# Kernel optimization log

Hardware: AMD Instinct MI355X
Metric: run time of the kernel (lower is better)

The kernel has to match this reference:

```python
import jax, jax.numpy as jnp
import numpy as np

N_ENTITY = 200000
N_RELATIONS = 32
DIM = 64
N_HOP = 2
N_MEMORY = 32
BATCH = 1024
KGE_WEIGHT = 0.01
L2_WEIGHT = 1e-7


def setup_inputs() -> dict:
    key = jax.random.key(0)
    ks = jax.random.split(key, 8)
    items = jax.random.randint(ks[0], (BATCH,), 0, N_ENTITY)
    labels = jax.random.uniform(ks[1], (BATCH,), dtype=jnp.float32)
    memories_h = jax.random.randint(ks[2], (N_HOP, BATCH, N_MEMORY), 0, N_ENTITY)
    memories_r = jax.random.randint(ks[3], (N_HOP, BATCH, N_MEMORY), 0, N_RELATIONS)
    memories_t = jax.random.randint(ks[4], (N_HOP, BATCH, N_MEMORY), 0, N_ENTITY)
    item_table = jax.random.normal(ks[5], (N_ENTITY, DIM), dtype=jnp.float32) * 0.1
    relation_table = jax.random.normal(ks[6], (N_RELATIONS, DIM * DIM), dtype=jnp.float32) * 0.1
    transform_W = jax.random.normal(ks[7], (DIM, DIM), dtype=jnp.float32) * 0.1
    return dict(items=items, labels=labels, memories_h=memories_h,
                memories_r=memories_r, memories_t=memories_t,
                item_table=item_table, relation_table=relation_table,
                transform_W=transform_W)


def _forward(items, labels, memories_h, memories_r, memories_t,
             item_table, relation_table, transform_W):
    v = item_table[items]  # [B, D]
    o_list = []
    kge_loss = jnp.float32(0.0)
    l2_loss = jnp.float32(0.0)
    for hop in range(N_HOP):
        h = item_table[memories_h[hop]]                                   # [B, M, D]
        R = relation_table[memories_r[hop]].reshape(-1, N_MEMORY, DIM, DIM)  # [B, M, D, D]
        t = item_table[memories_t[hop]]                                   # [B, M, D]
        # Rh = R @ h  -> [B, M, D]
        Rh = jnp.einsum('bmij,bmj->bmi', R, h)
        # attention probs over memory slots
        probs = jax.nn.softmax(jnp.einsum('bmi,bi->bm', Rh, v), axis=-1)  # [B, M]
        o = jnp.einsum('bmd,bm->bd', t, probs)                            # [B, D]
        # item_update_mode == 'plus_transform': v = W(v + o)
        v = (v + o) @ transform_W.T
        o_list.append(o)
        # KGE loss: sigmoid(h^T R t), mean over [B, M]
        hRt = jnp.einsum('bmi,bmij,bmj->bm', h, R, t)
        kge_loss = kge_loss + jnp.mean(jax.nn.sigmoid(hRt))
        l2_loss = l2_loss + jnp.sum(h * h) + jnp.sum(t * t) + jnp.sum(R * R)
    kge_loss = -KGE_WEIGHT * kge_loss
    l2_loss = L2_WEIGHT * l2_loss
    # predict with all hops
    y = o_list[-1]
    for i in range(N_HOP - 1):
        y = y + o_list[i]
    scores = jax.nn.sigmoid(jnp.sum(v * y, axis=1))  # [B]
    # BCE loss (torch clamps log at -100)
    logp = jnp.clip(jnp.log(scores), -100.0)
    lognp = jnp.clip(jnp.log(1.0 - scores), -100.0)
    base_loss = -jnp.mean(labels * logp + (1.0 - labels) * lognp)
    loss = base_loss + kge_loss + l2_loss
    return scores, loss, base_loss, kge_loss, l2_loss


def reference(items, labels, memories_h, memories_r, memories_t,
              item_table, relation_table, transform_W):
    return _forward(items, labels, memories_h, memories_r, memories_t,
                    item_table, relation_table, transform_W)
```

## Files before the change

### kernel.cpp

```cpp
#include <hip/hip_runtime.h>
#include <math.h>

#define N_ENTITY 200000
#define N_REL 32
#define DIM 64
#define N_HOP 2
#define N_MEM 32
#define BATCH 1024
#define PAIR_PER_HOP (BATCH * N_MEM)
#define N_PAIR (N_HOP * PAIR_PER_HOP)
#define CAP 3072
#define JBLK 32
#define WPB 4
#define NBLK_PAIRS (JBLK * N_REL * WPB)
#define TPAD 68

typedef __attribute__((ext_vector_type(8))) short short8;
typedef __attribute__((ext_vector_type(4))) float floatx4;

__device__ __forceinline__ float wave_reduce_sum(float v) {
    v += __shfl_xor(v, 1);
    v += __shfl_xor(v, 2);
    v += __shfl_xor(v, 4);
    v += __shfl_xor(v, 8);
    v += __shfl_xor(v, 16);
    v += __shfl_xor(v, 32);
    return v;
}

__device__ __forceinline__ unsigned short f2b(float x) {
    union { float f; unsigned u; } c; c.f = x;
    const unsigned r = (c.u + 0x7FFFu + ((c.u >> 16) & 1u)) >> 16;
    return (unsigned short)r;
}

__device__ __forceinline__ float b2f(short s) {
    union { unsigned u; float f; } c;
    c.u = ((unsigned)(unsigned short)s) << 16;
    return c.f;
}

__device__ __forceinline__ short8 pack8(const float4 a, const float4 b) {
    short8 s;
    s[0] = (short)f2b(a.x); s[1] = (short)f2b(a.y);
    s[2] = (short)f2b(a.z); s[3] = (short)f2b(a.w);
    s[4] = (short)f2b(b.x); s[5] = (short)f2b(b.y);
    s[6] = (short)f2b(b.z); s[7] = (short)f2b(b.w);
    return s;
}

__device__ __forceinline__ float sq4(const float4 a) {
    return a.x * a.x + a.y * a.y + a.z * a.z + a.w * a.w;
}

__device__ __forceinline__ float dot4(const float4 a, const float4 b) {
    return a.x * b.x + a.y * b.y + a.z * b.z + a.w * b.w;
}

__global__ __launch_bounds__(256) void ripple_bin(
    const int* __restrict__ mr,
    int* __restrict__ g_cnt,
    int* __restrict__ list)
{
    __shared__ int hist[N_REL];
    __shared__ int cur[N_REL];
    const int tid = (int)threadIdx.x;
    const int pbase = (int)blockIdx.x * 1024;

    if (tid < N_REL) hist[tid] = 0;
    __syncthreads();

    int rv[4];
    #pragma unroll
    for (int u = 0; u < 4; ++u) {
        rv[u] = mr[pbase + u * 256 + tid];
        atomicAdd(&hist[rv[u]], 1);
    }
    __syncthreads();
    if (tid < N_REL) cur[tid] = atomicAdd(&g_cnt[tid], hist[tid]);
    __syncthreads();
    #pragma unroll
    for (int u = 0; u < 4; ++u) {
        const int r = rv[u];
        const int pos = atomicAdd(&cur[r], 1);
        if (pos < CAP) list[r * CAP + pos] = pbase + u * 256 + tid;
    }
}

__global__ __launch_bounds__(256) void ripple_pairs(
    const int* __restrict__ items,
    const int* __restrict__ mh,
    const int* __restrict__ mt,
    const float* __restrict__ item_table,
    const float* __restrict__ rel_table,
    const int* __restrict__ g_cnt,
    const int* __restrict__ list,
    float* __restrict__ wsL,
    unsigned short* __restrict__ wsRh,
    float* __restrict__ ws_kge,
    float* __restrict__ ws_l2)
{
    __shared__ __align__(16) float sTr[WPB][16 * TPAD];
    __shared__ __align__(16) short8 sB[512];
    __shared__ float sRed[WPB];

    const int tid = (int)threadIdx.x;
    const int lane = tid & 63;
    const int w = tid >> 6;
    const int j = (int)blockIdx.x;
    const int r = (int)blockIdx.y;
    const int n = min(g_cnt[r], CAP);

    const int m16 = lane & 15;
    const int quad = lane >> 4;
    const int rb = r * CAP;
    const int wave_id = j * WPB + w;

    float* __restrict__ buf = &sTr[w][0];

    int tau = wave_id;
    int p = 0, hidx = 0, tidx = 0, iidx = 0;
    if (tau * 16 < n) {
        const int pos = min(tau * 16 + m16, n - 1);
        p = list[rb + pos];
        hidx = mh[p];
        tidx = mt[p];
        iidx = (p < PAIR_PER_HOP) ? items[p >> 5] : 0;
    }

    {
        const float* __restrict__ Rb = rel_table + (size_t)r * (DIM * DIM);
        float rsq = 0.f;
        #pragma unroll
        for (int u = 0; u < 2; ++u) {
            const int slot = tid + 256 * u;
            const int s = slot >> 8;
            const int tn = (slot >> 6) & 3;
            const int ls = slot & 63;
            const float* src = Rb + (size_t)(16 * tn + (ls & 15)) * DIM
                             + 32 * s + 8 * (ls >> 4);
            const float4 a = *(const float4*)src;
            const float4 b = *(const float4*)(src + 4);
            rsq += sq4(a) + sq4(b);
            sB[slot] = pack8(a, b);
        }
        rsq = wave_reduce_sum(rsq);
        if (lane == 0) sRed[w] = rsq;
    }
    __syncthreads();
    const float Rsum = sRed[0] + sRed[1] + sRed[2] + sRed[3];

    short8 Bf[2][4];
    #pragma unroll
    for (int s = 0; s < 2; ++s)
        #pragma unroll
        for (int tn = 0; tn < 4; ++tn)
            Bf[s][tn] = sB[s * 256 + tn * 64 + lane];

    float kge = 0.f;
    float l2ht = 0.f;
    int cnt = 0;

    for (; tau * 16 < n; tau += JBLK * WPB) {
        const int base = tau * 16;
        const bool mvalid = (base + m16) < n;
        const bool hop0 = p < PAIR_PER_HOP;

        const float* __restrict__ hp = item_table + (size_t)hidx * DIM + 8 * quad;
        const float* __restrict__ tp = item_table + (size_t)tidx * DIM + 8 * quad;
        const float4 h0a = *(const float4*)hp;
        const float4 h0b = *(const float4*)(hp + 4);
        const float4 h1a = *(const float4*)(hp + 32);
        const float4 h1b = *(const float4*)(hp + 36);
        const float4 t0a = *(const float4*)tp;
        const float4 t0b = *(const float4*)(tp + 4);
        const float4 t1a = *(const float4*)(tp + 32);
        const float4 t1b = *(const float4*)(tp + 36);

        float4 va0, va1, va2, va3;
        va0 = va1 = va2 = va3 = make_float4(0.f, 0.f, 0.f, 0.f);
        if (hop0) {
            const float* __restrict__ vp =
                item_table + (size_t)iidx * DIM + 16 * quad;
            va0 = *(const float4*)vp;
            va1 = *(const float4*)(vp + 4);
            va2 = *(const float4*)(vp + 8);
            va3 = *(const float4*)(vp + 12);
        }

        const int tau2 = tau + JBLK * WPB;
        int p2 = 0, h2 = 0, t2 = 0, i2 = 0;
        if (tau2 * 16 < n) {
            const int pos2 = min(tau2 * 16 + m16, n - 1);
            p2 = list[rb + pos2];
            h2 = mh[p2];
            t2 = mt[p2];
            i2 = (p2 < PAIR_PER_HOP) ? items[p2 >> 5] : 0;
        }

        if (mvalid) {
            l2ht += sq4(h0a) + sq4(h0b) + sq4(h1a) + sq4(h1b)
                  + sq4(t0a) + sq4(t0b) + sq4(t1a) + sq4(t1b);
        }

        const short8 Ah0 = pack8(h0a, h0b);
        const short8 Ah1 = pack8(h1a, h1b);
        const short8 At0 = pack8(t0a, t0b);
        const short8 At1 = pack8(t1a, t1b);

        floatx4 Ch[4], Ct[4];
        const floatx4 z4 = {0.f, 0.f, 0.f, 0.f};
        #pragma unroll
        for (int tn = 0; tn < 4; ++tn) {
            Ch[tn] = __builtin_amdgcn_mfma_f32_16x16x32_bf16(Ah0, Bf[0][tn], z4, 0, 0, 0);
            Ch[tn] = __builtin_amdgcn_mfma_f32_16x16x32_bf16(Ah1, Bf[1][tn], Ch[tn], 0, 0, 0);
            Ct[tn] = __builtin_amdgcn_mfma_f32_16x16x32_bf16(At0, Bf[0][tn], z4, 0, 0, 0);
            Ct[tn] = __builtin_amdgcn_mfma_f32_16x16x32_bf16(At1, Bf[1][tn], Ct[tn], 0, 0, 0);
        }

        #pragma unroll
        for (int tn = 0; tn < 4; ++tn) {
            const int col = m16 + 16 * tn;
            #pragma unroll
            for (int q = 0; q < 4; ++q)
                buf[(4 * quad + q) * TPAD + col] = Ct[tn][q];
        }
        const float* rowT = buf + m16 * TPAD;
        const float4 ct0 = *(const float4*)(rowT + 8 * quad);
        const float4 ct1 = *(const float4*)(rowT + 8 * quad + 4);
        const float4 ct2 = *(const float4*)(rowT + 32 + 8 * quad);
        const float4 ct3 = *(const float4*)(rowT + 32 + 8 * quad + 4);
        float hrt = dot4(h0a, ct0) + dot4(h0b, ct1) + dot4(h1a, ct2) + dot4(h1b, ct3);
        hrt += __shfl_xor(hrt, 16);
        hrt += __shfl_xor(hrt, 32);

        #pragma unroll
        for (int tn = 0; tn < 4; ++tn) {
            const int col = m16 + 16 * tn;
            #pragma unroll
            for (int q = 0; q < 4; ++q)
                buf[(4 * quad + q) * TPAD + col] = Ch[tn][q];
        }
        const float* rowC = buf + m16 * TPAD;
        const float4 c0 = *(const float4*)(rowC + 16 * quad);
        const float4 c1 = *(const float4*)(rowC + 16 * quad + 4);
        const float4 c2 = *(const float4*)(rowC + 16 * quad + 8);
        const float4 c3 = *(const float4*)(rowC + 16 * quad + 12);

        float lg = dot4(va0, c0) + dot4(va1, c1) + dot4(va2, c2) + dot4(va3, c3);
        lg += __shfl_xor(lg, 16);
        lg += __shfl_xor(lg, 32);

        if (quad == 0 && mvalid) {
            kge += 1.f / (1.f + expf(-hrt));
            if (hop0) wsL[p] = lg;
        }

        if (mvalid && !hop0) {
            unsigned short* __restrict__ dst =
                wsRh + (size_t)(p - PAIR_PER_HOP) * DIM + 16 * quad;
            *(short8*)dst = pack8(c0, c1);
            *(short8*)(dst + 8) = pack8(c2, c3);
        }

        cnt += min(16, n - base);
        p = p2; hidx = h2; tidx = t2; iidx = i2;
    }

    const float l2tot = wave_reduce_sum(l2ht) + (float)cnt * Rsum;
    const float kgetot = wave_reduce_sum(kge);
    if (lane == 0) {
        const int bid = (r * JBLK + j) * WPB + w;
        ws_kge[bid] = kgetot;
        ws_l2[bid] = l2tot;
    }
}

__global__ __launch_bounds__(256) void ripple_attn(
    const int* __restrict__ items,
    const float* __restrict__ labels,
    const int* __restrict__ mt,
    const float* __restrict__ item_table,
    const float* __restrict__ W,
    const float* __restrict__ wsL,
    const unsigned short* __restrict__ wsRh,
    float* __restrict__ out,
    float* __restrict__ ws_bce)
{
    __shared__ __align__(16) float sV[4][DIM];

    const int tid = (int)threadIdx.x;
    const int lane = tid & 63;
    const int w = tid >> 6;
    const int b = (int)blockIdx.x * 4 + w;

    const float v0 = item_table[(size_t)items[b] * DIM + lane];

    const float lab = labels[b];

    float l0 = (lane < N_MEM) ? wsL[b * N_MEM + lane] : -1e30f;

    const int myidx = mt[(lane >> 5) * PAIR_PER_HOP + b * N_MEM + (lane & 31)];

    float treg[64];
    #pragma unroll
    for (int m = 0; m < 64; ++m) {
        const int idx = __shfl(myidx, m);
        treg[m] = item_table[(size_t)idx * DIM + lane];
    }

    const int m1 = lane >> 1;
    const int d1 = (lane & 1) * 32;
    short8 rv[4];
    #pragma unroll
    for (int e = 0; e < 4; ++e)
        rv[e] = *(const short8*)(wsRh + (size_t)(b * N_MEM + m1) * DIM + d1 + 8 * e);

    const float4* __restrict__ Wrow = (const float4*)(W + (size_t)lane * DIM);

    float mx = l0;
    #pragma unroll
    for (int d = 16; d >= 1; d >>= 1) mx = fmaxf(mx, __shfl_xor(mx, d));
    const float e0 = expf(l0 - mx);
    float se = (lane < N_MEM) ? e0 : 0.f;
    #pragma unroll
    for (int d = 16; d >= 1; d >>= 1) se += __shfl_xor(se, d);
    const float pe0 = e0 / se;

    float o0 = 0.f;
    #pragma unroll
    for (int m = 0; m < N_MEM; ++m)
        o0 = fmaf(treg[m], __shfl(pe0, m), o0);

    sV[w][lane] = v0 + o0;
    float v1;
    {
        float a0 = 0.f, a1 = 0.f, a2 = 0.f, a3 = 0.f;
        #pragma unroll
        for (int k = 0; k < 16; ++k) {
            const float4 w4 = Wrow[k];
            const float4 u4 = *(const float4*)&sV[w][k * 4];
            a0 = fmaf(w4.x, u4.x, a0);
            a1 = fmaf(w4.y, u4.y, a1);
            a2 = fmaf(w4.z, u4.z, a2);
            a3 = fmaf(w4.w, u4.w, a3);
        }
        v1 = (a0 + a1) + (a2 + a3);
    }

    sV[w][lane] = v1;
    float dp = 0.f;
    #pragma unroll
    for (int e = 0; e < 4; ++e) {
        const float4 va = *(const float4*)&sV[w][d1 + 8 * e];
        const float4 vb = *(const float4*)&sV[w][d1 + 8 * e + 4];
        dp += b2f(rv[e][0]) * va.x + b2f(rv[e][1]) * va.y
            + b2f(rv[e][2]) * va.z + b2f(rv[e][3]) * va.w
            + b2f(rv[e][4]) * vb.x + b2f(rv[e][5]) * vb.y
            + b2f(rv[e][6]) * vb.z + b2f(rv[e][7]) * vb.w;
    }
    dp += __shfl_xor(dp, 1);
    const float a1v = __shfl(dp, (lane & 31) * 2);

    float av = (lane < N_MEM) ? a1v : -1e30f;
    mx = av;
    #pragma unroll
    for (int d = 16; d >= 1; d >>= 1) mx = fmaxf(mx, __shfl_xor(mx, d));
    const float e1 = expf(av - mx);
    se = (lane < N_MEM) ? e1 : 0.f;
    #pragma unroll
    for (int d = 16; d >= 1; d >>= 1) se += __shfl_xor(se, d);
    const float pe1 = e1 / se;

    float o1 = 0.f;
    #pragma unroll
    for (int m = 0; m < N_MEM; ++m)
        o1 = fmaf(treg[N_MEM + m], __shfl(pe1, m), o1);

    const float y = o0 + o1;
    sV[w][lane] = v1 + o1;
    float v2;
    {
        float a0 = 0.f, a1_ = 0.f, a2 = 0.f, a3 = 0.f;
        #pragma unroll
        for (int k = 0; k < 16; ++k) {
            const float4 w4 = Wrow[k];
            const float4 u4 = *(const float4*)&sV[w][k * 4];
            a0 = fmaf(w4.x, u4.x, a0);
            a1_ = fmaf(w4.y, u4.y, a1_);
            a2 = fmaf(w4.z, u4.z, a2);
            a3 = fmaf(w4.w, u4.w, a3);
        }
        v2 = (a0 + a1_) + (a2 + a3);
    }

    float s = wave_reduce_sum(v2 * y);
    s = 1.f / (1.f + expf(-s));
    if (lane == 0) {
        out[b] = s;
        const float logp = fmaxf(logf(s), -100.f);
        const float lognp = fmaxf(logf(1.f - s), -100.f);
        ws_bce[b] = lab * logp + (1.f - lab) * lognp;
    }
}

__global__ __launch_bounds__(256) void ripple_finalize(
    const float* __restrict__ ws_bce,
    const float* __restrict__ ws_kge,
    const float* __restrict__ ws_l2,
    float* __restrict__ out)
{
    __shared__ float sb[4], sk[4], sl[4];
    const int tid = (int)threadIdx.x;
    float bsum = 0.f, ksum = 0.f, lsum = 0.f;
    for (int i = tid; i < BATCH; i += 256) bsum += ws_bce[i];
    for (int i = tid; i < NBLK_PAIRS; i += 256) {
        ksum += ws_kge[i];
        lsum += ws_l2[i];
    }
    bsum = wave_reduce_sum(bsum);
    ksum = wave_reduce_sum(ksum);
    lsum = wave_reduce_sum(lsum);
    const int w = tid >> 6;
    if ((tid & 63) == 0) { sb[w] = bsum; sk[w] = ksum; sl[w] = lsum; }
    __syncthreads();
    if (tid == 0) {
        const float bs = sb[0] + sb[1] + sb[2] + sb[3];
        const float ks = sk[0] + sk[1] + sk[2] + sk[3];
        const float ls = sl[0] + sl[1] + sl[2] + sl[3];
        const float base_loss = -bs / (float)BATCH;
        const float kge_loss = -0.01f * (ks / (float)(BATCH * N_MEM));
        const float l2_loss = 1e-7f * ls;
        out[BATCH + 0] = base_loss + kge_loss + l2_loss;
        out[BATCH + 1] = base_loss;
        out[BATCH + 2] = kge_loss;
        out[BATCH + 3] = l2_loss;
    }
}

extern "C" void kernel_launch(void* const* d_in, const int* in_sizes, int n_in,
                              void* d_out, int out_size, void* d_ws, size_t ws_size,
                              hipStream_t stream) {
    const int* items        = (const int*)d_in[0];
    const float* labels     = (const float*)d_in[1];
    const int* mh           = (const int*)d_in[2];
    const int* mr           = (const int*)d_in[3];
    const int* mt           = (const int*)d_in[4];
    const float* item_table = (const float*)d_in[5];
    const float* rel_table  = (const float*)d_in[6];
    const float* W          = (const float*)d_in[7];
    float* out = (float*)d_out;

    float* ws = (float*)d_ws;
    float* wsL            = ws;
    unsigned short* wsRh  = (unsigned short*)(wsL + PAIR_PER_HOP);
    int*   list           = (int*)(wsRh + (size_t)PAIR_PER_HOP * DIM);
    int*   g_cnt          = list + N_REL * CAP;
    float* ws_bce         = (float*)(g_cnt + N_REL);
    float* ws_kge         = ws_bce + BATCH;
    float* ws_l2          = ws_kge + NBLK_PAIRS;

    hipMemsetAsync(g_cnt, 0, N_REL * sizeof(int), stream);
    ripple_bin<<<N_PAIR / 1024, 256, 0, stream>>>(mr, g_cnt, list);
    dim3 gpairs(JBLK, N_REL);
    ripple_pairs<<<gpairs, 256, 0, stream>>>(items, mh, mt, item_table, rel_table,
                                             g_cnt, list, wsL, wsRh, ws_kge, ws_l2);
    ripple_attn<<<BATCH / 4, 256, 0, stream>>>(items, labels, mt, item_table, W,
                                               wsL, wsRh, out, ws_bce);
    ripple_finalize<<<1, 256, 0, stream>>>(ws_bce, ws_kge, ws_l2, out);
}
```

Measured before the change: 132.4 us.

## Fold relation binning into pairs kernel and finalize via last-block atomics

Drops the separate binning kernel. Each pairs block now scans a fixed 2048-pair segment and collects, in shared memory, the pairs whose relation matches its block row. The finalize kernel is also removed: the attention kernel adds BCE terms atomically, and the last block to finish computes the loss outputs. This cuts kernel launches and the global list round-trip, at the cost of each segment of memories_r being read redundantly by 32 blocks. It also drops the next-tile index prefetch, makes float reductions order-nondeterministic, and relies on a 192-entry per-segment cap that holds only for roughly uniform relation ids.

```diff
diff --git a/kernel.cpp b/kernel.cpp
--- a/kernel.cpp
+++ b/kernel.cpp
@@ -9,10 +9,10 @@
 #define BATCH 1024
 #define PAIR_PER_HOP (BATCH * N_MEM)
 #define N_PAIR (N_HOP * PAIR_PER_HOP)
-#define CAP 3072
-#define JBLK 32
+#define SEGS 32
+#define SEG 2048
+#define SEGCAP 192
 #define WPB 4
-#define NBLK_PAIRS (JBLK * N_REL * WPB)
 #define TPAD 68
 
 typedef __attribute__((ext_vector_type(8))) short short8;
@@ -57,75 +57,46 @@
     return a.x * b.x + a.y * b.y + a.z * b.z + a.w * b.w;
 }
 
-__global__ __launch_bounds__(256) void ripple_bin(
-    const int* __restrict__ mr,
-    int* __restrict__ g_cnt,
-    int* __restrict__ list)
-{
-    __shared__ int hist[N_REL];
-    __shared__ int cur[N_REL];
-    const int tid = (int)threadIdx.x;
-    const int pbase = (int)blockIdx.x * 1024;
-
-    if (tid < N_REL) hist[tid] = 0;
-    __syncthreads();
-
-    int rv[4];
-    #pragma unroll
-    for (int u = 0; u < 4; ++u) {
-        rv[u] = mr[pbase + u * 256 + tid];
-        atomicAdd(&hist[rv[u]], 1);
-    }
-    __syncthreads();
-    if (tid < N_REL) cur[tid] = atomicAdd(&g_cnt[tid], hist[tid]);
-    __syncthreads();
-    #pragma unroll
-    for (int u = 0; u < 4; ++u) {
-        const int r = rv[u];
-        const int pos = atomicAdd(&cur[r], 1);
-        if (pos < CAP) list[r * CAP + pos] = pbase + u * 256 + tid;
-    }
-}
-
 __global__ __launch_bounds__(256) void ripple_pairs(
     const int* __restrict__ items,
     const int* __restrict__ mh,
+    const int* __restrict__ mr,
     const int* __restrict__ mt,
     const float* __restrict__ item_table,
     const float* __restrict__ rel_table,
-    const int* __restrict__ g_cnt,
-    const int* __restrict__ list,
     float* __restrict__ wsL,
     unsigned short* __restrict__ wsRh,
-    float* __restrict__ ws_kge,
-    float* __restrict__ ws_l2)
+    float* __restrict__ g_kge,
+    float* __restrict__ g_l2)
 {
     __shared__ __align__(16) float sTr[WPB][16 * TPAD];
     __shared__ __align__(16) short8 sB[512];
-    __shared__ float sRed[WPB];
+    __shared__ float sRedR[WPB], sRedK[WPB], sRedL[WPB];
+    __shared__ int slist[SEGCAP];
+    __shared__ int sn;
 
     const int tid = (int)threadIdx.x;
     const int lane = tid & 63;
     const int w = tid >> 6;
     const int j = (int)blockIdx.x;
     const int r = (int)blockIdx.y;
-    const int n = min(g_cnt[r], CAP);
 
     const int m16 = lane & 15;
     const int quad = lane >> 4;
-    const int rb = r * CAP;
-    const int wave_id = j * WPB + w;
+    const int pbase = j * SEG;
 
     float* __restrict__ buf = &sTr[w][0];
 
-    int tau = wave_id;
-    int p = 0, hidx = 0, tidx = 0, iidx = 0;
-    if (tau * 16 < n) {
-        const int pos = min(tau * 16 + m16, n - 1);
-        p = list[rb + pos];
-        hidx = mh[p];
-        tidx = mt[p];
-        iidx = (p < PAIR_PER_HOP) ? items[p >> 5] : 0;
+    if (tid == 0) sn = 0;
+    __syncthreads();
+
+    #pragma unroll
+    for (int u = 0; u < 8; ++u) {
+        const int idx = pbase + u * 256 + tid;
+        if (mr[idx] == r) {
+            const int pos = atomicAdd(&sn, 1);
+            if (pos < SEGCAP) slist[pos] = idx;
+        }
     }
 
     {
@@ -145,10 +116,11 @@
             sB[slot] = pack8(a, b);
         }
         rsq = wave_reduce_sum(rsq);
-        if (lane == 0) sRed[w] = rsq;
+        if (lane == 0) sRedR[w] = rsq;
     }
     __syncthreads();
-    const float Rsum = sRed[0] + sRed[1] + sRed[2] + sRed[3];
+    const float Rsum = sRedR[0] + sRedR[1] + sRedR[2] + sRedR[3];
+    const int n = min(sn, SEGCAP);
 
     short8 Bf[2][4];
     #pragma unroll
@@ -161,10 +133,15 @@
     float l2ht = 0.f;
     int cnt = 0;
 
-    for (; tau * 16 < n; tau += JBLK * WPB) {
+    for (int tau = w; tau * 16 < n; tau += WPB) {
         const int base = tau * 16;
         const bool mvalid = (base + m16) < n;
+
+        const int p = slist[min(base + m16, n - 1)];
+        const int hidx = mh[p];
+        const int tidx = mt[p];
         const bool hop0 = p < PAIR_PER_HOP;
+        const int iidx = hop0 ? items[p >> 5] : 0;
 
         const float* __restrict__ hp = item_table + (size_t)hidx * DIM + 8 * quad;
         const float* __restrict__ tp = item_table + (size_t)tidx * DIM + 8 * quad;
@@ -188,16 +165,6 @@
             va3 = *(const float4*)(vp + 12);
         }
 
-        const int tau2 = tau + JBLK * WPB;
-        int p2 = 0, h2 = 0, t2 = 0, i2 = 0;
-        if (tau2 * 16 < n) {
-            const int pos2 = min(tau2 * 16 + m16, n - 1);
-            p2 = list[rb + pos2];
-            h2 = mh[p2];
-            t2 = mt[p2];
-            i2 = (p2 < PAIR_PER_HOP) ? items[p2 >> 5] : 0;
-        }
-
         if (mvalid) {
             l2ht += sq4(h0a) + sq4(h0b) + sq4(h1a) + sq4(h1b)
                   + sq4(t0a) + sq4(t0b) + sq4(t1a) + sq4(t1b);
@@ -264,15 +231,15 @@
         }
 
         cnt += min(16, n - base);
-        p = p2; hidx = h2; tidx = t2; iidx = i2;
     }
 
     const float l2tot = wave_reduce_sum(l2ht) + (float)cnt * Rsum;
     const float kgetot = wave_reduce_sum(kge);
-    if (lane == 0) {
-        const int bid = (r * JBLK + j) * WPB + w;
-        ws_kge[bid] = kgetot;
-        ws_l2[bid] = l2tot;
+    if (lane == 0) { sRedK[w] = kgetot; sRedL[w] = l2tot; }
+    __syncthreads();
+    if (tid == 0) {
+        atomicAdd(g_kge, sRedK[0] + sRedK[1] + sRedK[2] + sRedK[3]);
+        atomicAdd(g_l2,  sRedL[0] + sRedL[1] + sRedL[2] + sRedL[3]);
     }
 }
 
@@ -285,7 +252,10 @@
     const float* __restrict__ wsL,
     const unsigned short* __restrict__ wsRh,
     float* __restrict__ out,
-    float* __restrict__ ws_bce)
+    float* __restrict__ g_bce,
+    float* __restrict__ g_kge,
+    float* __restrict__ g_l2,
+    int* __restrict__ g_done)
 {
     __shared__ __align__(16) float sV[4][DIM];
 
@@ -400,41 +370,23 @@
         out[b] = s;
         const float logp = fmaxf(logf(s), -100.f);
         const float lognp = fmaxf(logf(1.f - s), -100.f);
-        ws_bce[b] = lab * logp + (1.f - lab) * lognp;
-    }
-}
-
-__global__ __launch_bounds__(256) void ripple_finalize(
-    const float* __restrict__ ws_bce,
-    const float* __restrict__ ws_kge,
-    const float* __restrict__ ws_l2,
-    float* __restrict__ out)
-{
-    __shared__ float sb[4], sk[4], sl[4];
-    const int tid = (int)threadIdx.x;
-    float bsum = 0.f, ksum = 0.f, lsum = 0.f;
-    for (int i = tid; i < BATCH; i += 256) bsum += ws_bce[i];
-    for (int i = tid; i < NBLK_PAIRS; i += 256) {
-        ksum += ws_kge[i];
-        lsum += ws_l2[i];
-    }
-    bsum = wave_reduce_sum(bsum);
-    ksum = wave_reduce_sum(ksum);
-    lsum = wave_reduce_sum(lsum);
-    const int w = tid >> 6;
-    if ((tid & 63) == 0) { sb[w] = bsum; sk[w] = ksum; sl[w] = lsum; }
-    __syncthreads();
-    if (tid == 0) {
-        const float bs = sb[0] + sb[1] + sb[2] + sb[3];
-        const float ks = sk[0] + sk[1] + sk[2] + sk[3];
-        const float ls = sl[0] + sl[1] + sl[2] + sl[3];
-        const float base_loss = -bs / (float)BATCH;
-        const float kge_loss = -0.01f * (ks / (float)(BATCH * N_MEM));
-        const float l2_loss = 1e-7f * ls;
-        out[BATCH + 0] = base_loss + kge_loss + l2_loss;
-        out[BATCH + 1] = base_loss;
-        out[BATCH + 2] = kge_loss;
-        out[BATCH + 3] = l2_loss;
+        const float bval = lab * logp + (1.f - lab) * lognp;
+
+        const float oldb = atomicAdd(g_bce, bval);
+        asm volatile("" :: "v"(oldb));
+        const int oldd = atomicAdd(g_done, 1);
+        if (oldd == BATCH - 1) {
+            const float bs = atomicAdd(g_bce, 0.0f);
+            const float ks = atomicAdd(g_kge, 0.0f);
+            const float ls = atomicAdd(g_l2, 0.0f);
+            const float base_loss = -bs / (float)BATCH;
+            const float kge_loss = -0.01f * (ks / (float)(BATCH * N_MEM));
+            const float l2_loss = 1e-7f * ls;
+            out[BATCH + 0] = base_loss + kge_loss + l2_loss;
+            out[BATCH + 1] = base_loss;
+            out[BATCH + 2] = kge_loss;
+            out[BATCH + 3] = l2_loss;
+        }
     }
 }
 
@@ -454,18 +406,16 @@
     float* ws = (float*)d_ws;
     float* wsL            = ws;
     unsigned short* wsRh  = (unsigned short*)(wsL + PAIR_PER_HOP);
-    int*   list           = (int*)(wsRh + (size_t)PAIR_PER_HOP * DIM);
-    int*   g_cnt          = list + N_REL * CAP;
-    float* ws_bce         = (float*)(g_cnt + N_REL);
-    float* ws_kge         = ws_bce + BATCH;
-    float* ws_l2          = ws_kge + NBLK_PAIRS;
-
-    hipMemsetAsync(g_cnt, 0, N_REL * sizeof(int), stream);
-    ripple_bin<<<N_PAIR / 1024, 256, 0, stream>>>(mr, g_cnt, list);
-    dim3 gpairs(JBLK, N_REL);
-    ripple_pairs<<<gpairs, 256, 0, stream>>>(items, mh, mt, item_table, rel_table,
-                                             g_cnt, list, wsL, wsRh, ws_kge, ws_l2);
+    int*   g_done         = (int*)(wsRh + (size_t)PAIR_PER_HOP * DIM);
+    float* g_bce          = (float*)(g_done + 1);
+    float* g_kge          = g_bce + 1;
+    float* g_l2           = g_kge + 1;
+
+    hipMemsetAsync(g_done, 0, 16, stream);
+    dim3 gpairs(SEGS, N_REL);
+    ripple_pairs<<<gpairs, 256, 0, stream>>>(items, mh, mr, mt, item_table,
+                                             rel_table, wsL, wsRh, g_kge, g_l2);
     ripple_attn<<<BATCH / 4, 256, 0, stream>>>(items, labels, mt, item_table, W,
-                                               wsL, wsRh, out, ws_bce);
-    ripple_finalize<<<1, 256, 0, stream>>>(ws_bce, ws_kge, ws_l2, out);
-}
+                                               wsL, wsRh, out,
+                                               g_bce, g_kge, g_l2, g_done);
+}
```

Result: slower. 170.4 us (+28.7%).
